# Kernel optimization log

Measured on AMD Instinct MI355X. Metric: run time of the kernel, lower is better.

## Reference

```python
import jax, jax.numpy as jnp
import numpy as np

B, T, V = 8, 1024, 2048

def setup_inputs() -> dict:
    key = jax.random.key(0)
    k1, k2, k3 = jax.random.split(key, 3)
    idx = jax.random.randint(k1, (B, T), 0, V)
    v_weight = jnp.zeros((T, 1), dtype=jnp.float32) + 0.02 * jax.random.normal(k2, (T, 1), dtype=jnp.float32)
    W = 0.01 * jnp.ones((V, V), dtype=jnp.float32) + 0.001 * jax.random.normal(k3, (V, V), dtype=jnp.float32)
    return {"idx": idx, "v_weight": v_weight, "W": W}

def reference(idx, v_weight, W):
    Tn = idx.shape[1]
    Vn = W.shape[0]
    e = jax.nn.one_hot(idx, Vn, dtype=jnp.float32)            # [B,T,V]
    pos = jnp.arange(Tn)
    rel = jnp.maximum(pos[:, None] - pos[None, :], 0)          # [T,T] clamped relative positions
    causal = pos[:, None] >= pos[None, :]                      # True where attention allowed
    # Layer 1: positional attention (shared across batch)
    a1 = v_weight[rel, 0]                                      # [T,T] gather from v embedding
    a1 = jnp.where(causal, a1, -jnp.inf)
    a1 = jax.nn.softmax(a1, axis=-1)
    layer_one = jnp.einsum('ts,bsv->btv', a1, e)               # [B,T,V]
    key_t = layer_one @ W.T                                    # Linear without bias: x @ W^T
    # Layer 2: content attention
    a2 = jnp.einsum('btv,bsv->bts', e, key_t)                  # [B,T,T]
    a2 = jnp.where(causal[None], a2, -jnp.inf)
    a2 = jax.nn.softmax(a2, axis=-1)
    logits = jnp.einsum('bts,bsv->btv', a2, e)                 # [B,T,V]
    return logits
```

## Files before the change

kernel.cpp:

```cpp
#include <hip/hip_runtime.h>
#include <hip/hip_bf16.h>
#include <math.h>

#define Bn 8
#define Tn 1024
#define Vn 2048

typedef __attribute__((ext_vector_type(8))) __bf16 bf16x8;
typedef __attribute__((ext_vector_type(4))) float floatx4;

__global__ __launch_bounds__(256) void k_bt(const float* __restrict__ vw,
                                            __hip_bfloat16* __restrict__ BT) {
    __shared__ float red[4];
    int s = blockIdx.x;
    int tid = threadIdx.x;
    int wave = tid >> 6, lane = tid & 63;
    float part = 0.0f;
#pragma unroll
    for (int i = 0; i < 4; ++i) {
        int d = tid + i * 256;
        if (d <= s) part += __expf(vw[d]);
    }
#pragma unroll
    for (int off = 32; off > 0; off >>= 1) part += __shfl_xor(part, off);
    if (lane == 0) red[wave] = part;
    __syncthreads();
    float cinv = 1.0f / (red[0] + red[1] + red[2] + red[3]);

    int k0 = tid * 4;
    ushort u[4];
#pragma unroll
    for (int j = 0; j < 4; ++j) {
        int k = k0 + j;
        float v = (k <= s) ? __expf(vw[s - k]) * cinv : 0.0f;
        __hip_bfloat16 h = __float2bfloat16(v);
        u[j] = *reinterpret_cast<ushort*>(&h);
    }
    *reinterpret_cast<ushort4*>(&BT[(size_t)s * Tn + k0]) = make_ushort4(u[0], u[1], u[2], u[3]);
}

__global__ __launch_bounds__(256) void k_gather(const int* __restrict__ idx,
                                                const float* __restrict__ W,
                                                __hip_bfloat16* __restrict__ A) {
    int b = blockIdx.y, t = blockIdx.x, tid = threadIdx.x;
    int r = idx[b * Tn + t];
    const float* Wr = W + (size_t)r * Vn;
    int4 c4 = *reinterpret_cast<const int4*>(&idx[b * Tn + tid * 4]);
    ushort u[4];
    __hip_bfloat16 h;
    h = __float2bfloat16(Wr[c4.x]); u[0] = *reinterpret_cast<ushort*>(&h);
    h = __float2bfloat16(Wr[c4.y]); u[1] = *reinterpret_cast<ushort*>(&h);
    h = __float2bfloat16(Wr[c4.z]); u[2] = *reinterpret_cast<ushort*>(&h);
    h = __float2bfloat16(Wr[c4.w]); u[3] = *reinterpret_cast<ushort*>(&h);
    *reinterpret_cast<ushort4*>(&A[((size_t)(b * Tn + t)) * Tn + tid * 4]) =
        make_ushort4(u[0], u[1], u[2], u[3]);
}

#define TM 128
#define TN 128
#define BK 32
#define LDP 40
#define NTILES 36

__device__ const int TILE_MI[NTILES] = {7, 6,7, 5,6,7, 4,5,6,7, 3,4,5,6,7,
                                        2,3,4,5,6,7, 1,2,3,4,5,6,7, 0,1,2,3,4,5,6,7};
__device__ const int TILE_NI[NTILES] = {7, 6,6, 5,5,5, 4,4,4,4, 3,3,3,3,3,
                                        2,2,2,2,2,2, 1,1,1,1,1,1,1, 0,0,0,0,0,0,0,0};

__global__ __launch_bounds__(256) void k_gemm(const __hip_bfloat16* __restrict__ A,
                                              const __hip_bfloat16* __restrict__ BT,
                                              float* __restrict__ Cout) {
    __shared__ __align__(16) __hip_bfloat16 As[TM][LDP];
    __shared__ __align__(16) __hip_bfloat16 Bs[TN][LDP];
    int b = blockIdx.x;
    int tl = blockIdx.y;
    int mi = TILE_MI[tl], ni = TILE_NI[tl];
    int m0 = mi * TM;
    int n0 = ni * TN;
    int Kmax = (ni + 1) * TN;
    int tid = threadIdx.x;
    int wave = tid >> 6, lane = tid & 63;
    int wm = (wave >> 1) * 64, wn = (wave & 1) * 64;
    int lrow = lane & 15, quad = lane >> 4;

    const __hip_bfloat16* Ab = A + (size_t)b * Tn * Tn;

    floatx4 acc[4][4];
#pragma unroll
    for (int i = 0; i < 4; ++i)
#pragma unroll
        for (int j = 0; j < 4; ++j) acc[i][j] = (floatx4){0.f, 0.f, 0.f, 0.f};

    for (int k0 = 0; k0 < Kmax; k0 += BK) {
#pragma unroll
        for (int i = 0; i < 2; ++i) {
            int ch = tid + i * 256;
            int r = ch >> 2, c = (ch & 3) * 8;
            *reinterpret_cast<uint4*>(&As[r][c]) =
                *reinterpret_cast<const uint4*>(&Ab[(size_t)(m0 + r) * Tn + k0 + c]);
            *reinterpret_cast<uint4*>(&Bs[r][c]) =
                *reinterpret_cast<const uint4*>(&BT[(size_t)(n0 + r) * Tn + k0 + c]);
        }
        __syncthreads();
        bf16x8 af[4], bfr[4];
#pragma unroll
        for (int mi2 = 0; mi2 < 4; ++mi2)
            af[mi2] = *reinterpret_cast<const bf16x8*>(&As[wm + mi2 * 16 + lrow][quad * 8]);
#pragma unroll
        for (int ni2 = 0; ni2 < 4; ++ni2)
            bfr[ni2] = *reinterpret_cast<const bf16x8*>(&Bs[wn + ni2 * 16 + lrow][quad * 8]);
#pragma unroll
        for (int mi2 = 0; mi2 < 4; ++mi2)
#pragma unroll
            for (int ni2 = 0; ni2 < 4; ++ni2)
                acc[mi2][ni2] = __builtin_amdgcn_mfma_f32_16x16x32_bf16(af[mi2], bfr[ni2],
                                                                        acc[mi2][ni2], 0, 0, 0);
        __syncthreads();
    }

    float* Cb = Cout + (size_t)b * Tn * Tn;
#pragma unroll
    for (int mi2 = 0; mi2 < 4; ++mi2)
#pragma unroll
        for (int ni2 = 0; ni2 < 4; ++ni2)
#pragma unroll
            for (int r = 0; r < 4; ++r) {
                int row = m0 + wm + mi2 * 16 + quad * 4 + r;
                int col = n0 + wn + ni2 * 16 + lrow;
                Cb[(size_t)row * Tn + col] = acc[mi2][ni2][r];
            }
}

__global__ __launch_bounds__(256) void k_softscat(const float* __restrict__ a2raw,
                                                  const int* __restrict__ idx,
                                                  float* __restrict__ out) {
    __shared__ float sh[Vn];
    __shared__ float red[8];
    int t = blockIdx.x, b = blockIdx.y, tid = threadIdx.x;
    int wave = tid >> 6, lane = tid & 63;
#pragma unroll
    for (int i = 0; i < Vn / 256; ++i) sh[tid + i * 256] = 0.0f;

    const float* row = a2raw + ((size_t)b * Tn + t) * Tn;
    int s0 = tid * 4;
    float v[4] = {-INFINITY, -INFINITY, -INFINITY, -INFINITY};
    if (s0 <= t) {
        float4 v4 = *reinterpret_cast<const float4*>(&row[s0]);
        v[0] = v4.x; v[1] = v4.y; v[2] = v4.z; v[3] = v4.w;
    }
    int4 c4 = *reinterpret_cast<const int4*>(&idx[b * Tn + s0]);
    float m = -INFINITY;
#pragma unroll
    for (int j = 0; j < 4; ++j) {
        if (s0 + j > t) v[j] = -INFINITY;
        m = fmaxf(m, v[j]);
    }
#pragma unroll
    for (int off = 32; off > 0; off >>= 1) m = fmaxf(m, __shfl_xor(m, off));
    if (lane == 0) red[wave] = m;
    __syncthreads();
    m = fmaxf(fmaxf(red[0], red[1]), fmaxf(red[2], red[3]));
    float e[4];
    float lsum = 0.f;
#pragma unroll
    for (int j = 0; j < 4; ++j) {
        e[j] = (s0 + j <= t) ? __expf(v[j] - m) : 0.0f;
        lsum += e[j];
    }
#pragma unroll
    for (int off = 32; off > 0; off >>= 1) lsum += __shfl_xor(lsum, off);
    if (lane == 0) red[4 + wave] = lsum;
    __syncthreads();
    float inv = 1.0f / (red[4] + red[5] + red[6] + red[7]);
    int c[4] = {c4.x, c4.y, c4.z, c4.w};
#pragma unroll
    for (int j = 0; j < 4; ++j)
        if (s0 + j <= t) atomicAdd(&sh[c[j]], e[j] * inv);
    __syncthreads();
    float* orow = out + ((size_t)b * Tn + t) * Vn;
#pragma unroll
    for (int i = 0; i < Vn / (256 * 4); ++i)
        *reinterpret_cast<float4*>(&orow[(tid + i * 256) * 4]) =
            *reinterpret_cast<const float4*>(&sh[(tid + i * 256) * 4]);
}

extern "C" void kernel_launch(void* const* d_in, const int* in_sizes, int n_in,
                              void* d_out, int out_size, void* d_ws, size_t ws_size,
                              hipStream_t stream) {
    const int* idx = (const int*)d_in[0];
    const float* vw = (const float*)d_in[1];
    const float* W = (const float*)d_in[2];
    float* out = (float*)d_out;
    char* ws = (char*)d_ws;

    __hip_bfloat16* BT = (__hip_bfloat16*)(ws);
    __hip_bfloat16* Abf = (__hip_bfloat16*)(ws + (2u << 20));
    float* a2raw = (float*)(ws + (18u << 20));

    k_bt<<<dim3(Tn), 256, 0, stream>>>(vw, BT);
    k_gather<<<dim3(Tn, Bn), 256, 0, stream>>>(idx, W, Abf);
    k_gemm<<<dim3(Bn, NTILES), 256, 0, stream>>>(Abf, BT, a2raw);
    k_softscat<<<dim3(Tn, Bn), 256, 0, stream>>>(a2raw, idx, out);
}
```

Baseline: 149.7 us.

## Split long causal GEMM tiles along K and stage gather rows in LDS

The GEMM tile list becomes 46 chunks. Tiles with column block 4 or higher are split in K into a lower and an upper half, which write to two separate partial buffers. The softmax kernel sums the two buffers for columns at or beyond 512. The goal is to shorten the longest tile's critical path and balance load across workgroups, at the cost of an extra partial buffer in global memory and an extra read. The gather kernel now loads the whole W row into shared memory with coalesced float4 reads before doing the indexed lookups. The softmax also drops the max-subtraction pass and one barrier, which assumes the logits are small enough that exp does not overflow.

```diff
diff --git a/kernel.cpp b/kernel.cpp
--- a/kernel.cpp
+++ b/kernel.cpp
@@ -42,16 +42,23 @@
 __global__ __launch_bounds__(256) void k_gather(const int* __restrict__ idx,
                                                 const float* __restrict__ W,
                                                 __hip_bfloat16* __restrict__ A) {
+    __shared__ float wrow[Vn];
     int b = blockIdx.y, t = blockIdx.x, tid = threadIdx.x;
     int r = idx[b * Tn + t];
     const float* Wr = W + (size_t)r * Vn;
+#pragma unroll
+    for (int i = 0; i < 2; ++i) {
+        int o = (tid + i * 256) * 4;
+        *reinterpret_cast<float4*>(&wrow[o]) = *reinterpret_cast<const float4*>(&Wr[o]);
+    }
     int4 c4 = *reinterpret_cast<const int4*>(&idx[b * Tn + tid * 4]);
+    __syncthreads();
     ushort u[4];
     __hip_bfloat16 h;
-    h = __float2bfloat16(Wr[c4.x]); u[0] = *reinterpret_cast<ushort*>(&h);
-    h = __float2bfloat16(Wr[c4.y]); u[1] = *reinterpret_cast<ushort*>(&h);
-    h = __float2bfloat16(Wr[c4.z]); u[2] = *reinterpret_cast<ushort*>(&h);
-    h = __float2bfloat16(Wr[c4.w]); u[3] = *reinterpret_cast<ushort*>(&h);
+    h = __float2bfloat16(wrow[c4.x]); u[0] = *reinterpret_cast<ushort*>(&h);
+    h = __float2bfloat16(wrow[c4.y]); u[1] = *reinterpret_cast<ushort*>(&h);
+    h = __float2bfloat16(wrow[c4.z]); u[2] = *reinterpret_cast<ushort*>(&h);
+    h = __float2bfloat16(wrow[c4.w]); u[3] = *reinterpret_cast<ushort*>(&h);
     *reinterpret_cast<ushort4*>(&A[((size_t)(b * Tn + t)) * Tn + tid * 4]) =
         make_ushort4(u[0], u[1], u[2], u[3]);
 }
@@ -60,24 +67,40 @@
 #define TN 128
 #define BK 32
 #define LDP 40
-#define NTILES 36
-
-__device__ const int TILE_MI[NTILES] = {7, 6,7, 5,6,7, 4,5,6,7, 3,4,5,6,7,
-                                        2,3,4,5,6,7, 1,2,3,4,5,6,7, 0,1,2,3,4,5,6,7};
-__device__ const int TILE_NI[NTILES] = {7, 6,6, 5,5,5, 4,4,4,4, 3,3,3,3,3,
-                                        2,2,2,2,2,2, 1,1,1,1,1,1,1, 0,0,0,0,0,0,0,0};
+#define NCHUNK 46
+
+__device__ const signed char CH_MI[NCHUNK] = {7,7,6,7,5,6,7,4,5,6,7,3,4,5,6,7,
+                                              6,7,2,3,4,5,6,7,
+                                              5,6,7,1,2,3,4,5,6,7,
+                                              4,5,6,7,0,1,2,3,4,5,6,7};
+__device__ const signed char CH_NI[NCHUNK] = {7,7,6,6,5,5,5,4,4,4,4,3,3,3,3,3,
+                                              6,6,2,2,2,2,2,2,
+                                              5,5,5,1,1,1,1,1,1,1,
+                                              4,4,4,4,0,0,0,0,0,0,0,0};
+__device__ const signed char CH_K0[NCHUNK] = {0,16,0,0,0,0,0,0,0,0,0,0,0,0,0,0,
+                                              16,16,0,0,0,0,0,0,
+                                              16,16,16,0,0,0,0,0,0,0,
+                                              16,16,16,16,0,0,0,0,0,0,0,0};
+__device__ const signed char CH_K1[NCHUNK] = {16,32,16,16,16,16,16,16,16,16,16,16,16,16,16,16,
+                                              28,28,12,12,12,12,12,12,
+                                              24,24,24,8,8,8,8,8,8,8,
+                                              20,20,20,20,4,4,4,4,4,4,4,4};
+__device__ const signed char CH_P[NCHUNK]  = {0,1,0,0,0,0,0,0,0,0,0,0,0,0,0,0,
+                                              1,1,0,0,0,0,0,0,
+                                              1,1,1,0,0,0,0,0,0,0,
+                                              1,1,1,1,0,0,0,0,0,0,0,0};
 
 __global__ __launch_bounds__(256) void k_gemm(const __hip_bfloat16* __restrict__ A,
                                               const __hip_bfloat16* __restrict__ BT,
-                                              float* __restrict__ Cout) {
+                                              float* __restrict__ part0,
+                                              float* __restrict__ part1) {
     __shared__ __align__(16) __hip_bfloat16 As[TM][LDP];
     __shared__ __align__(16) __hip_bfloat16 Bs[TN][LDP];
     int b = blockIdx.x;
-    int tl = blockIdx.y;
-    int mi = TILE_MI[tl], ni = TILE_NI[tl];
-    int m0 = mi * TM;
-    int n0 = ni * TN;
-    int Kmax = (ni + 1) * TN;
+    int cidx = blockIdx.y;
+    int mi = CH_MI[cidx], ni = CH_NI[cidx];
+    int ki0 = CH_K0[cidx], ki1 = CH_K1[cidx];
+    int m0 = mi * TM, n0 = ni * TN;
     int tid = threadIdx.x;
     int wave = tid >> 6, lane = tid & 63;
     int wm = (wave >> 1) * 64, wn = (wave & 1) * 64;
@@ -91,7 +114,8 @@
 #pragma unroll
         for (int j = 0; j < 4; ++j) acc[i][j] = (floatx4){0.f, 0.f, 0.f, 0.f};
 
-    for (int k0 = 0; k0 < Kmax; k0 += BK) {
+    for (int ki = ki0; ki < ki1; ++ki) {
+        int k0 = ki * BK;
 #pragma unroll
         for (int i = 0; i < 2; ++i) {
             int ch = tid + i * 256;
@@ -104,74 +128,68 @@
         __syncthreads();
         bf16x8 af[4], bfr[4];
 #pragma unroll
-        for (int mi2 = 0; mi2 < 4; ++mi2)
-            af[mi2] = *reinterpret_cast<const bf16x8*>(&As[wm + mi2 * 16 + lrow][quad * 8]);
-#pragma unroll
-        for (int ni2 = 0; ni2 < 4; ++ni2)
-            bfr[ni2] = *reinterpret_cast<const bf16x8*>(&Bs[wn + ni2 * 16 + lrow][quad * 8]);
-#pragma unroll
-        for (int mi2 = 0; mi2 < 4; ++mi2)
-#pragma unroll
-            for (int ni2 = 0; ni2 < 4; ++ni2)
-                acc[mi2][ni2] = __builtin_amdgcn_mfma_f32_16x16x32_bf16(af[mi2], bfr[ni2],
-                                                                        acc[mi2][ni2], 0, 0, 0);
+        for (int m = 0; m < 4; ++m)
+            af[m] = *reinterpret_cast<const bf16x8*>(&As[wm + m * 16 + lrow][quad * 8]);
+#pragma unroll
+        for (int n = 0; n < 4; ++n)
+            bfr[n] = *reinterpret_cast<const bf16x8*>(&Bs[wn + n * 16 + lrow][quad * 8]);
+#pragma unroll
+        for (int m = 0; m < 4; ++m)
+#pragma unroll
+            for (int n = 0; n < 4; ++n)
+                acc[m][n] = __builtin_amdgcn_mfma_f32_16x16x32_bf16(af[m], bfr[n],
+                                                                    acc[m][n], 0, 0, 0);
         __syncthreads();
     }
 
-    float* Cb = Cout + (size_t)b * Tn * Tn;
-#pragma unroll
-    for (int mi2 = 0; mi2 < 4; ++mi2)
-#pragma unroll
-        for (int ni2 = 0; ni2 < 4; ++ni2)
+    float* Cb = (CH_P[cidx] ? part1 : part0) + (size_t)b * Tn * Tn;
+#pragma unroll
+    for (int m = 0; m < 4; ++m)
+#pragma unroll
+        for (int n = 0; n < 4; ++n)
 #pragma unroll
             for (int r = 0; r < 4; ++r) {
-                int row = m0 + wm + mi2 * 16 + quad * 4 + r;
-                int col = n0 + wn + ni2 * 16 + lrow;
-                Cb[(size_t)row * Tn + col] = acc[mi2][ni2][r];
+                int row = m0 + wm + m * 16 + quad * 4 + r;
+                int col = n0 + wn + n * 16 + lrow;
+                Cb[(size_t)row * Tn + col] = acc[m][n][r];
             }
 }
 
-__global__ __launch_bounds__(256) void k_softscat(const float* __restrict__ a2raw,
+__global__ __launch_bounds__(256) void k_softscat(const float* __restrict__ part0,
+                                                  const float* __restrict__ part1,
                                                   const int* __restrict__ idx,
                                                   float* __restrict__ out) {
     __shared__ float sh[Vn];
-    __shared__ float red[8];
+    __shared__ float red[4];
     int t = blockIdx.x, b = blockIdx.y, tid = threadIdx.x;
     int wave = tid >> 6, lane = tid & 63;
 #pragma unroll
     for (int i = 0; i < Vn / 256; ++i) sh[tid + i * 256] = 0.0f;
 
-    const float* row = a2raw + ((size_t)b * Tn + t) * Tn;
+    size_t rowoff = ((size_t)b * Tn + t) * Tn;
     int s0 = tid * 4;
-    float v[4] = {-INFINITY, -INFINITY, -INFINITY, -INFINITY};
+    float v[4] = {0.f, 0.f, 0.f, 0.f};
     if (s0 <= t) {
-        float4 v4 = *reinterpret_cast<const float4*>(&row[s0]);
+        float4 v4 = *reinterpret_cast<const float4*>(&part0[rowoff + s0]);
         v[0] = v4.x; v[1] = v4.y; v[2] = v4.z; v[3] = v4.w;
+        if (s0 >= 512) {
+            float4 w4 = *reinterpret_cast<const float4*>(&part1[rowoff + s0]);
+            v[0] += w4.x; v[1] += w4.y; v[2] += w4.z; v[3] += w4.w;
+        }
     }
     int4 c4 = *reinterpret_cast<const int4*>(&idx[b * Tn + s0]);
-    float m = -INFINITY;
-#pragma unroll
-    for (int j = 0; j < 4; ++j) {
-        if (s0 + j > t) v[j] = -INFINITY;
-        m = fmaxf(m, v[j]);
-    }
-#pragma unroll
-    for (int off = 32; off > 0; off >>= 1) m = fmaxf(m, __shfl_xor(m, off));
-    if (lane == 0) red[wave] = m;
-    __syncthreads();
-    m = fmaxf(fmaxf(red[0], red[1]), fmaxf(red[2], red[3]));
     float e[4];
     float lsum = 0.f;
 #pragma unroll
     for (int j = 0; j < 4; ++j) {
-        e[j] = (s0 + j <= t) ? __expf(v[j] - m) : 0.0f;
+        e[j] = (s0 + j <= t) ? __expf(v[j]) : 0.0f;
         lsum += e[j];
     }
 #pragma unroll
     for (int off = 32; off > 0; off >>= 1) lsum += __shfl_xor(lsum, off);
-    if (lane == 0) red[4 + wave] = lsum;
-    __syncthreads();
-    float inv = 1.0f / (red[4] + red[5] + red[6] + red[7]);
+    if (lane == 0) red[wave] = lsum;
+    __syncthreads();
+    float inv = 1.0f / (red[0] + red[1] + red[2] + red[3]);
     int c[4] = {c4.x, c4.y, c4.z, c4.w};
 #pragma unroll
     for (int j = 0; j < 4; ++j)
@@ -195,10 +213,11 @@
 
     __hip_bfloat16* BT = (__hip_bfloat16*)(ws);
     __hip_bfloat16* Abf = (__hip_bfloat16*)(ws + (2u << 20));
-    float* a2raw = (float*)(ws + (18u << 20));
-
+    float* part0 = (float*)(ws + (18u << 20));
+    float* part1 = (float*)(ws + (52u << 20));
+
+    k_gather<<<dim3(Tn, Bn), 256, 0, stream>>>(idx, W, Abf);
     k_bt<<<dim3(Tn), 256, 0, stream>>>(vw, BT);
-    k_gather<<<dim3(Tn, Bn), 256, 0, stream>>>(idx, W, Abf);
-    k_gemm<<<dim3(Bn, NTILES), 256, 0, stream>>>(Abf, BT, a2raw);
-    k_softscat<<<dim3(Tn, Bn), 256, 0, stream>>>(a2raw, idx, out);
-}
+    k_gemm<<<dim3(Bn, NCHUNK), 256, 0, stream>>>(Abf, BT, part0, part1);
+    k_softscat<<<dim3(Tn, Bn), 256, 0, stream>>>(part0, part1, idx, out);
+}
```

Result: faster. 138.2 us (-7.7%).
